# Kernel optimization log

Measured on AMD Instinct MI355X. Metric: run time of the kernel, lower is better.

## Reference

```python
import jax, jax.numpy as jnp
import numpy as np

B, C, H, W = 4, 128, 128, 128
HEADS, DHEAD = 8, C // 8
N = H * W
NEG_SLOPE = 0.2
LN_EPS = 1e-5


def _build_grid_edges(h, w):
    # 3x3 neighborhood including self (matches the torch double loop),
    # then append N extra self loops (add_self_loops in the module).
    rows, cols = [], []
    for r in range(h):
        for c in range(w):
            idx = r * w + c
            for dr in (-1, 0, 1):
                for dc in (-1, 0, 1):
                    nr, nc = r + dr, c + dc
                    if 0 <= nr < h and 0 <= nc < w:
                        rows.append(idx)
                        cols.append(nr * w + nc)
    rows += list(range(h * w))
    cols += list(range(h * w))
    return np.asarray(rows, np.int32), np.asarray(cols, np.int32)

_SRC_NP, _DST_NP = _build_grid_edges(H, W)  # PyG: messages flow src -> dst
SRC = jnp.asarray(_SRC_NP)
DST = jnp.asarray(_DST_NP)


def setup_inputs() -> dict:
    key = jax.random.key(0)
    ks = jax.random.split(key, 7)
    s_lin = 1.0 / np.sqrt(C)
    return {
        "x": jax.random.normal(ks[0], (B, C, H, W), jnp.float32),
        "W_lin": jax.random.normal(ks[1], (C, HEADS * DHEAD), jnp.float32) * s_lin,
        "att_src": jax.random.normal(ks[2], (HEADS, DHEAD), jnp.float32) * s_lin,
        "att_dst": jax.random.normal(ks[3], (HEADS, DHEAD), jnp.float32) * s_lin,
        "bias": jnp.zeros((C,), jnp.float32),
        "gamma": jnp.ones((C,), jnp.float32),
        "beta": jnp.zeros((C,), jnp.float32),
    }


def _gat_forward(x, W_lin, att_src, att_dst, bias, gamma, beta):
    b = x.shape[0]
    x_nodes = x.reshape(b, C, N).transpose(0, 2, 1)            # [B,N,C]
    xp = (x_nodes @ W_lin).reshape(b, N, HEADS, DHEAD)          # [B,N,H,D]
    a_src = jnp.einsum('bnhd,hd->bnh', xp, att_src)             # [B,N,H]
    a_dst = jnp.einsum('bnhd,hd->bnh', xp, att_dst)
    score = jax.nn.leaky_relu(a_src[:, SRC] + a_dst[:, DST], NEG_SLOPE)  # [B,E,H]

    def seg_softmax(s):  # [E,H] softmax over edges grouped by DST
        m = jax.ops.segment_max(s, DST, num_segments=N)
        e = jnp.exp(s - m[DST])
        den = jax.ops.segment_sum(e, DST, num_segments=N)
        return e / den[DST]

    alpha = jax.vmap(seg_softmax)(score)                        # [B,E,H]
    msg = xp[:, SRC] * alpha[..., None]                         # [B,E,H,D]
    agg = jax.vmap(lambda m: jax.ops.segment_sum(m, DST, num_segments=N))(msg)
    out = agg.reshape(b, N, C) + bias                           # GATConv bias
    out = jax.nn.elu(out)
    # LayerNorm over channel dim
    mu = out.mean(-1, keepdims=True)
    var = out.var(-1, keepdims=True)
    out = (out - mu) * jax.lax.rsqrt(var + LN_EPS) * gamma + beta
    return out.transpose(0, 2, 1).reshape(b, C, H, W)


def reference(x, W_lin, att_src, att_dst, bias, gamma, beta):
    return _gat_forward(x, W_lin, att_src, att_dst, bias, gamma, beta)
```

## Files before the change

kernel.cpp:

```cpp
#include <hip/hip_runtime.h>
#include <stdint.h>

#define BATCH  4
#define CCH    128
#define GRID_H 128
#define GRID_W 128
#define NNODE  (GRID_H*GRID_W)
#define NHEAD  8
#define DH     16
#define WPAD   68
#define WROWS  144

typedef __attribute__((ext_vector_type(8))) short short8;
typedef __attribute__((ext_vector_type(4))) float f32x4;
typedef __attribute__((ext_vector_type(4))) unsigned u32x4;

__device__ inline unsigned short f2bf(float f){
    unsigned u = __float_as_uint(f);
    return (unsigned short)((u + 0x7FFFu + ((u >> 16) & 1u)) >> 16);
}
__device__ inline unsigned packbf(float a, float b){
    return (unsigned)f2bf(a) | ((unsigned)f2bf(b) << 16);
}
__device__ inline float bflo(unsigned u){ return __uint_as_float(u << 16); }
__device__ inline float bfhi(unsigned u){ return __uint_as_float(u & 0xFFFF0000u); }

__global__ void kW(const float* __restrict__ Wl, const float* __restrict__ attS,
                   const float* __restrict__ attD, unsigned* __restrict__ Wb)
{
    __shared__ float Wa[8][16];
    const int t = threadIdx.x;
    const int cbase = blockIdx.x * 8;
    if (t < 128){
        int cl = t >> 4, j = t & 15;
        const float* av = (j < 8 ? attS + j*DH : attD + (j-8)*DH);
        const float* wr = Wl + (size_t)(cbase + cl)*CCH + (j & 7)*DH;
        float s = 0.f;
        #pragma unroll
        for (int d = 0; d < DH; ++d) s += wr[d]*av[d];
        Wa[cl][j] = s;
    }
    __syncthreads();
    for (int it = 0; it < 3; ++it){
        int flat = it*256 + t;
        if (flat < 576){
            int k2l = flat / 144, co = flat % 144;
            int k2 = blockIdx.x*4 + k2l;
            float w0, w1;
            if (co < CCH){
                w0 = Wl[(size_t)(2*k2)*CCH + co];
                w1 = Wl[(size_t)(2*k2+1)*CCH + co];
            } else {
                w0 = Wa[2*k2l][co-CCH];
                w1 = Wa[2*k2l+1][co-CCH];
            }
            Wb[co*WPAD + k2] = packbf(w0, w1);
        }
    }
}

__global__ __launch_bounds__(256, 3) void kA(
    const float* __restrict__ x, const unsigned* __restrict__ Wbg,
    unsigned short* __restrict__ xpb, float* __restrict__ scb)
{
    __shared__ __align__(16) unsigned WbL[WROWS*WPAD];

    const int t  = threadIdx.x;
    const int b  = blockIdx.y;
    const int n0 = blockIdx.x * 128;

    #pragma unroll
    for (int it = 0; it < 10; ++it){
        int f4 = it*256 + t;
        if (f4 < (WROWS*WPAD)/4)
            *(u32x4*)(&WbL[f4*4]) = *(const u32x4*)(Wbg + (size_t)f4*4);
    }
    __syncthreads();

    const int w = t >> 6, lane = t & 63;
    const int col = lane & 15, q = lane >> 4;
    const float* xb = x + (size_t)b*CCH*NNODE;
    const int nA = n0 + (2*w+0)*16 + col;
    const int nB = n0 + (2*w+1)*16 + col;

    f32x4 acc[2][9];
    #pragma unroll
    for (int mi = 0; mi < 2; ++mi)
        #pragma unroll
        for (int ct = 0; ct < 9; ++ct) acc[mi][ct] = (f32x4)(0.f);

    float xrA[8], xrB[8], x2A[8], x2B[8];
    #pragma unroll
    for (int j = 0; j < 8; ++j){
        const size_t co = (size_t)(q*8 + j)*NNODE;
        xrA[j] = xb[co + nA];
        xrB[j] = xb[co + nB];
    }

    union U { u32x4 u; short8 s; };
    #pragma unroll
    for (int kc = 0; kc < 4; ++kc){
        if (kc < 3){
            #pragma unroll
            for (int j = 0; j < 8; ++j){
                const size_t co = (size_t)((kc+1)*32 + q*8 + j)*NNODE;
                x2A[j] = xb[co + nA];
                x2B[j] = xb[co + nB];
            }
        }
        U fa0, fa1;
        #pragma unroll
        for (int i = 0; i < 4; ++i){
            fa0.u[i] = packbf(xrA[2*i], xrA[2*i+1]);
            fa1.u[i] = packbf(xrB[2*i], xrB[2*i+1]);
        }
        const int kof = kc*16 + q*4;
        #pragma unroll
        for (int ct = 0; ct < 9; ++ct){
            U fb; fb.u = *(const u32x4*)(&WbL[(ct*16+col)*WPAD + kof]);
            acc[0][ct] = __builtin_amdgcn_mfma_f32_16x16x32_bf16(fa0.s, fb.s, acc[0][ct], 0, 0, 0);
            acc[1][ct] = __builtin_amdgcn_mfma_f32_16x16x32_bf16(fa1.s, fb.s, acc[1][ct], 0, 0, 0);
        }
        #pragma unroll
        for (int j = 0; j < 8; ++j){ xrA[j] = x2A[j]; xrB[j] = x2B[j]; }
    }

    unsigned short* xr = xpb + (size_t)b*NNODE*CCH;
    float*          sr = scb + (size_t)b*NNODE*16;
    const int sidx = (col < 8) ? 2*col : 2*(col-8)+1;
    #pragma unroll
    for (int mi = 0; mi < 2; ++mi){
        #pragma unroll
        for (int r = 0; r < 4; ++r){
            const int n = n0 + (2*w+mi)*16 + q*4 + r;
            #pragma unroll
            for (int ct = 0; ct < 8; ++ct)
                xr[(size_t)n*CCH + ct*16 + col] = f2bf(acc[mi][ct][r]);
            sr[(size_t)n*16 + sidx] = acc[mi][8][r];
        }
    }
}

__device__ inline void kb_issue(int n, const float2* __restrict__ scB,
                                const uint2* __restrict__ xvb, int h, int l2,
                                int* vm, float2 sc[9], uint2 xv[9])
{
    const int rr = n >> 7, cc = n & 127;
    const bool vU = rr > 0, vD = rr < GRID_H-1, vL = cc > 0, vR = cc < GRID_W-1;
    int m = 0;
    #pragma unroll
    for (int e = 0; e < 9; ++e){
        const int dr = e/3 - 1, dc = e%3 - 1;
        const bool vr_ = (dr < 0) ? vU : (dr > 0 ? vD : true);
        const bool vc_ = (dc < 0) ? vL : (dc > 0 ? vR : true);
        const bool v = vr_ && vc_;
        const int src = v ? (n + dr*GRID_W + dc) : n;
        m |= ((int)v) << e;
        sc[e] = scB[src*8 + h];
        xv[e] = xvb[(size_t)src*32 + l2];
    }
    *vm = m;
}

__global__ __launch_bounds__(256, 3) void kB(
    const unsigned short* __restrict__ xpb, const float* __restrict__ scb,
    const float* __restrict__ bias, const float* __restrict__ gamma,
    const float* __restrict__ beta, float* __restrict__ out)
{
    __shared__ float outT[CCH][65];
    const int t = threadIdx.x, w = t >> 6, lane = t & 63;
    const int h2 = lane >> 5, l2 = lane & 31;
    const int b  = blockIdx.y;
    const int n0 = blockIdx.x * 64;
    const uint2*  xvb = (const uint2*)(xpb + (size_t)b*NNODE*CCH);
    const float2* scB = (const float2*)(scb + (size_t)b*NNODE*16);
    const int h = l2 >> 2;
    const f32x4 bi = *(const f32x4*)(bias  + 4*l2);
    const f32x4 ga = *(const f32x4*)(gamma + 4*l2);
    const f32x4 be = *(const f32x4*)(beta  + 4*l2);

    float2 scP[2][9]; uint2 xvP[2][9]; int vmP[2];

    #define NODE(i) (n0 + w*16 + 2*(i) + h2)
    kb_issue(NODE(0), scB, xvb, h, l2, &vmP[0], scP[0], xvP[0]);

    #pragma unroll
    for (int ii = 0; ii < 4; ++ii){
        #pragma unroll
        for (int ph = 0; ph < 2; ++ph){
            const int i = 2*ii + ph;
            const int cur = i & 1;
            if (i + 1 < 8)
                kb_issue(NODE(i+1), scB, xvb, h, l2, &vmP[cur^1], scP[cur^1], xvP[cur^1]);

            const int vm = vmP[cur];
            const float2* sc = scP[cur];
            const uint2*  xv = xvP[cur];
            const int nl = w*16 + 2*i + h2;

            const float ad = sc[4].y;
            float s[9], mx = -1e30f;
            #pragma unroll
            for (int e = 0; e < 9; ++e){
                float sv = sc[e].x + ad;
                sv = fmaxf(sv, 0.2f*sv);
                s[e] = ((vm >> e) & 1) ? sv : -1e30f;
                mx = fmaxf(mx, s[e]);
            }
            float wt[9], den = 0.f;
            #pragma unroll
            for (int e = 0; e < 9; ++e){
                float ex = __expf(s[e] - mx);
                ex = ((vm >> e) & 1) ? ex : 0.f;
                wt[e] = ex; den += ex;
            }
            den += wt[4];
            const float inv = __builtin_amdgcn_rcpf(den);

            float a0 = 0.f, a1 = 0.f, a2 = 0.f, a3 = 0.f;
            #pragma unroll
            for (int e = 0; e < 9; ++e){
                float f = wt[e] * inv;
                if (e == 4) f += f;
                a0 += f * bflo(xv[e].x);
                a1 += f * bfhi(xv[e].x);
                a2 += f * bflo(xv[e].y);
                a3 += f * bfhi(xv[e].y);
            }

            float o0 = a0 + bi[0], o1 = a1 + bi[1], o2 = a2 + bi[2], o3 = a3 + bi[3];
            o0 = o0 > 0.f ? o0 : __expf(o0) - 1.f;
            o1 = o1 > 0.f ? o1 : __expf(o1) - 1.f;
            o2 = o2 > 0.f ? o2 : __expf(o2) - 1.f;
            o3 = o3 > 0.f ? o3 : __expf(o3) - 1.f;

            float sm = (o0 + o1) + (o2 + o3);
            float sq = o0*o0 + o1*o1 + o2*o2 + o3*o3;
            #pragma unroll
            for (int off = 1; off <= 16; off <<= 1){
                sm += __shfl_xor(sm, off, 64);
                sq += __shfl_xor(sq, off, 64);
            }
            const float mu  = sm * (1.f/128.f);
            float var = sq * (1.f/128.f) - mu*mu;
            var = var < 0.f ? 0.f : var;
            const float rstd = __builtin_amdgcn_rsqf(var + 1e-5f);
            outT[4*l2+0][nl] = (o0 - mu)*rstd*ga[0] + be[0];
            outT[4*l2+1][nl] = (o1 - mu)*rstd*ga[1] + be[1];
            outT[4*l2+2][nl] = (o2 - mu)*rstd*ga[2] + be[2];
            outT[4*l2+3][nl] = (o3 - mu)*rstd*ga[3] + be[3];
        }
    }
    #undef NODE
    __syncthreads();

    float* ob = out + (size_t)b*CCH*NNODE + n0;
    #pragma unroll
    for (int it = 0; it < 32; ++it){
        int c = it*4 + w;
        ob[(size_t)c*NNODE + lane] = outT[c][lane];
    }
}

extern "C" void kernel_launch(void* const* d_in, const int* in_sizes, int n_in,
                              void* d_out, int out_size, void* d_ws, size_t ws_size,
                              hipStream_t stream)
{
    const float* x    = (const float*)d_in[0];
    const float* Wl   = (const float*)d_in[1];
    const float* attS = (const float*)d_in[2];
    const float* attD = (const float*)d_in[3];
    const float* bias = (const float*)d_in[4];
    const float* gamma= (const float*)d_in[5];
    const float* beta = (const float*)d_in[6];
    float* out = (float*)d_out;

    unsigned short* xpb = (unsigned short*)d_ws;
    float*          scb = (float*)(xpb + (size_t)BATCH*NNODE*CCH);
    unsigned*       Wb  = (unsigned*)(scb + (size_t)BATCH*NNODE*16);

    kW<<<dim3(16), 256, 0, stream>>>(Wl, attS, attD, Wb);
    kA<<<dim3(NNODE/128, BATCH), 256, 0, stream>>>(x, Wb, xpb, scb);
    kB<<<dim3(NNODE/64, BATCH), 256, 0, stream>>>(xpb, scb, bias, gamma, beta, out);
}
```

Baseline: 117.6 us.

## Fold weight prep into projection kernel, switch to fp16 with packed FMA, remap blocks

Removes the separate weight-preparation kernel. Each projection block now computes the attention-folded weights and packs them to bf16 in shared memory with a hardware packed-convert instruction. The intermediate projection is stored as fp16 and aggregated with packed half2 FMAs, and source and destination scores go into separate arrays. Blocks are remapped so row groups interleave across XCDs, aiming for better L2 locality of neighbouring rows. This saves one launch and some ALU work, but every block redoes the weight preparation, and accumulating in fp16 reduces precision.

New measurement: 119.7 us. No clear change (+1.8%).

```diff
diff --git a/kernel.cpp b/kernel.cpp
--- a/kernel.cpp
+++ b/kernel.cpp
@@ -1,4 +1,5 @@
 #include <hip/hip_runtime.h>
+#include <hip/hip_fp16.h>
 #include <stdint.h>
 
 #define BATCH  4
@@ -15,65 +16,72 @@
 typedef __attribute__((ext_vector_type(4))) float f32x4;
 typedef __attribute__((ext_vector_type(4))) unsigned u32x4;
 
-__device__ inline unsigned short f2bf(float f){
-    unsigned u = __float_as_uint(f);
-    return (unsigned short)((u + 0x7FFFu + ((u >> 16) & 1u)) >> 16);
-}
 __device__ inline unsigned packbf(float a, float b){
-    return (unsigned)f2bf(a) | ((unsigned)f2bf(b) << 16);
-}
-__device__ inline float bflo(unsigned u){ return __uint_as_float(u << 16); }
-__device__ inline float bfhi(unsigned u){ return __uint_as_float(u & 0xFFFF0000u); }
-
-__global__ void kW(const float* __restrict__ Wl, const float* __restrict__ attS,
-                   const float* __restrict__ attD, unsigned* __restrict__ Wb)
-{
-    __shared__ float Wa[8][16];
-    const int t = threadIdx.x;
-    const int cbase = blockIdx.x * 8;
-    if (t < 128){
-        int cl = t >> 4, j = t & 15;
-        const float* av = (j < 8 ? attS + j*DH : attD + (j-8)*DH);
-        const float* wr = Wl + (size_t)(cbase + cl)*CCH + (j & 7)*DH;
-        float s = 0.f;
-        #pragma unroll
-        for (int d = 0; d < DH; ++d) s += wr[d]*av[d];
-        Wa[cl][j] = s;
-    }
-    __syncthreads();
-    for (int it = 0; it < 3; ++it){
-        int flat = it*256 + t;
-        if (flat < 576){
-            int k2l = flat / 144, co = flat % 144;
-            int k2 = blockIdx.x*4 + k2l;
-            float w0, w1;
-            if (co < CCH){
-                w0 = Wl[(size_t)(2*k2)*CCH + co];
-                w1 = Wl[(size_t)(2*k2+1)*CCH + co];
-            } else {
-                w0 = Wa[2*k2l][co-CCH];
-                w1 = Wa[2*k2l+1][co-CCH];
-            }
-            Wb[co*WPAD + k2] = packbf(w0, w1);
-        }
-    }
+    unsigned r;
+    asm("v_cvt_pk_bf16_f32 %0, %1, %2" : "=v"(r) : "v"(a), "v"(b));
+    return r;
+}
+__device__ inline unsigned packhf(float a, float b){
+    unsigned r;
+    asm("v_cvt_pkrtz_f16_f32 %0, %1, %2" : "=v"(r) : "v"(a), "v"(b));
+    return r;
 }
 
 __global__ __launch_bounds__(256, 3) void kA(
-    const float* __restrict__ x, const unsigned* __restrict__ Wbg,
-    unsigned short* __restrict__ xpb, float* __restrict__ scb)
+    const float* __restrict__ x,   const float* __restrict__ Wl,
+    const float* __restrict__ attS, const float* __restrict__ attD,
+    __half* __restrict__ xpb, float* __restrict__ scS, float* __restrict__ scD)
 {
     __shared__ __align__(16) unsigned WbL[WROWS*WPAD];
+    __shared__ __align__(16) float att2[2*CCH];
+    __shared__ float Wa[CCH][17];
 
     const int t  = threadIdx.x;
     const int b  = blockIdx.y;
-    const int n0 = blockIdx.x * 128;
-
-    #pragma unroll
-    for (int it = 0; it < 10; ++it){
-        int f4 = it*256 + t;
-        if (f4 < (WROWS*WPAD)/4)
-            *(u32x4*)(&WbL[f4*4]) = *(const u32x4*)(Wbg + (size_t)f4*4);
+    const int bx = blockIdx.x;
+    const int row = (bx & 7)*16 + (bx >> 3);
+    const int n0  = row * GRID_W;
+
+    att2[t] = (t < CCH) ? attS[t] : attD[t - CCH];
+    __syncthreads();
+
+    {
+        const int j = t & 15;
+        f32x4 av[4];
+        #pragma unroll
+        for (int d4 = 0; d4 < 4; ++d4) av[d4] = *(const f32x4*)&att2[j*16 + d4*4];
+        #pragma unroll
+        for (int it = 0; it < 8; ++it){
+            const int k = it*16 + (t >> 4);
+            const float* wr = Wl + (size_t)k*CCH + (j & 7)*16;
+            float s = 0.f;
+            #pragma unroll
+            for (int d4 = 0; d4 < 4; ++d4){
+                f32x4 wv = *(const f32x4*)(wr + d4*4);
+                s += wv[0]*av[d4][0] + wv[1]*av[d4][1] + wv[2]*av[d4][2] + wv[3]*av[d4][3];
+            }
+            Wa[k][j] = s;
+        }
+    }
+    __syncthreads();
+
+    {
+        const int k2 = t >> 2, cb = t & 3;
+        const float* r0 = Wl + (size_t)(2*k2)*CCH + cb*32;
+        const float* r1 = r0 + CCH;
+        #pragma unroll
+        for (int i4 = 0; i4 < 8; ++i4){
+            f32x4 a = *(const f32x4*)(r0 + i4*4);
+            f32x4 c = *(const f32x4*)(r1 + i4*4);
+            #pragma unroll
+            for (int u = 0; u < 4; ++u)
+                WbL[(cb*32 + i4*4 + u)*WPAD + k2] = packbf(a[u], c[u]);
+        }
+        #pragma unroll
+        for (int jj = 0; jj < 4; ++jj){
+            const int j = cb*4 + jj;
+            WbL[(CCH + j)*WPAD + k2] = packbf(Wa[2*k2][j], Wa[2*k2+1][j]);
+        }
     }
     __syncthreads();
 
@@ -125,9 +133,9 @@
         for (int j = 0; j < 8; ++j){ xrA[j] = x2A[j]; xrB[j] = x2B[j]; }
     }
 
-    unsigned short* xr = xpb + (size_t)b*NNODE*CCH;
-    float*          sr = scb + (size_t)b*NNODE*16;
-    const int sidx = (col < 8) ? 2*col : 2*(col-8)+1;
+    __half* xr = xpb + (size_t)b*NNODE*CCH;
+    float*  sS = scS + (size_t)b*NNODE*NHEAD;
+    float*  sD = scD + (size_t)b*NNODE*NHEAD;
     #pragma unroll
     for (int mi = 0; mi < 2; ++mi){
         #pragma unroll
@@ -135,15 +143,18 @@
             const int n = n0 + (2*w+mi)*16 + q*4 + r;
             #pragma unroll
             for (int ct = 0; ct < 8; ++ct)
-                xr[(size_t)n*CCH + ct*16 + col] = f2bf(acc[mi][ct][r]);
-            sr[(size_t)n*16 + sidx] = acc[mi][8][r];
-        }
-    }
-}
-
-__device__ inline void kb_issue(int n, const float2* __restrict__ scB,
+                xr[(size_t)n*CCH + ct*16 + col] = __float2half(acc[mi][ct][r]);
+            const float v = acc[mi][8][r];
+            if (col < 8) sS[(size_t)n*NHEAD + col]     = v;
+            else         sD[(size_t)n*NHEAD + col - 8] = v;
+        }
+    }
+}
+
+__device__ inline void kb_issue(int n, const float* __restrict__ scSb,
+                                const float* __restrict__ scDb,
                                 const uint2* __restrict__ xvb, int h, int l2,
-                                int* vm, float2 sc[9], uint2 xv[9])
+                                int* vm, float aS[9], float* aD, uint2 xv[9])
 {
     const int rr = n >> 7, cc = n & 127;
     const bool vU = rr > 0, vD = rr < GRID_H-1, vL = cc > 0, vR = cc < GRID_W-1;
@@ -156,14 +167,16 @@
         const bool v = vr_ && vc_;
         const int src = v ? (n + dr*GRID_W + dc) : n;
         m |= ((int)v) << e;
-        sc[e] = scB[src*8 + h];
+        aS[e] = scSb[src*NHEAD + h];
         xv[e] = xvb[(size_t)src*32 + l2];
     }
+    *aD = scDb[n*NHEAD + h];
     *vm = m;
 }
 
 __global__ __launch_bounds__(256, 3) void kB(
-    const unsigned short* __restrict__ xpb, const float* __restrict__ scb,
+    const __half* __restrict__ xpb, const float* __restrict__ scS,
+    const float* __restrict__ scD,
     const float* __restrict__ bias, const float* __restrict__ gamma,
     const float* __restrict__ beta, float* __restrict__ out)
 {
@@ -171,18 +184,23 @@
     const int t = threadIdx.x, w = t >> 6, lane = t & 63;
     const int h2 = lane >> 5, l2 = lane & 31;
     const int b  = blockIdx.y;
-    const int n0 = blockIdx.x * 64;
-    const uint2*  xvb = (const uint2*)(xpb + (size_t)b*NNODE*CCH);
-    const float2* scB = (const float2*)(scb + (size_t)b*NNODE*16);
+    const int bx = blockIdx.x;
+    const int xcd = bx & 7, rest = bx >> 3;
+    const int hlf = rest & 1, rowin = rest >> 1;
+    const int n0  = (xcd*16 + rowin)*GRID_W + hlf*64;
+
+    const uint2* xvb  = (const uint2*)(xpb + (size_t)b*NNODE*CCH);
+    const float* scSb = scS + (size_t)b*NNODE*NHEAD;
+    const float* scDb = scD + (size_t)b*NNODE*NHEAD;
     const int h = l2 >> 2;
     const f32x4 bi = *(const f32x4*)(bias  + 4*l2);
     const f32x4 ga = *(const f32x4*)(gamma + 4*l2);
     const f32x4 be = *(const f32x4*)(beta  + 4*l2);
 
-    float2 scP[2][9]; uint2 xvP[2][9]; int vmP[2];
+    float aSP[2][9]; uint2 xvP[2][9]; float aDP[2]; int vmP[2];
 
     #define NODE(i) (n0 + w*16 + 2*(i) + h2)
-    kb_issue(NODE(0), scB, xvb, h, l2, &vmP[0], scP[0], xvP[0]);
+    kb_issue(NODE(0), scSb, scDb, xvb, h, l2, &vmP[0], aSP[0], &aDP[0], xvP[0]);
 
     #pragma unroll
     for (int ii = 0; ii < 4; ++ii){
@@ -191,18 +209,19 @@
             const int i = 2*ii + ph;
             const int cur = i & 1;
             if (i + 1 < 8)
-                kb_issue(NODE(i+1), scB, xvb, h, l2, &vmP[cur^1], scP[cur^1], xvP[cur^1]);
+                kb_issue(NODE(i+1), scSb, scDb, xvb, h, l2,
+                         &vmP[cur^1], aSP[cur^1], &aDP[cur^1], xvP[cur^1]);
 
             const int vm = vmP[cur];
-            const float2* sc = scP[cur];
+            const float* aS = aSP[cur];
             const uint2*  xv = xvP[cur];
+            const float ad = aDP[cur];
             const int nl = w*16 + 2*i + h2;
 
-            const float ad = sc[4].y;
             float s[9], mx = -1e30f;
             #pragma unroll
             for (int e = 0; e < 9; ++e){
-                float sv = sc[e].x + ad;
+                float sv = aS[e] + ad;
                 sv = fmaxf(sv, 0.2f*sv);
                 s[e] = ((vm >> e) & 1) ? sv : -1e30f;
                 mx = fmaxf(mx, s[e]);
@@ -217,16 +236,20 @@
             den += wt[4];
             const float inv = __builtin_amdgcn_rcpf(den);
 
-            float a0 = 0.f, a1 = 0.f, a2 = 0.f, a3 = 0.f;
+            union HU { unsigned u; __half2 h; };
+            HU a01, a23; a01.u = 0u; a23.u = 0u;
             #pragma unroll
             for (int e = 0; e < 9; ++e){
                 float f = wt[e] * inv;
                 if (e == 4) f += f;
-                a0 += f * bflo(xv[e].x);
-                a1 += f * bfhi(xv[e].x);
-                a2 += f * bflo(xv[e].y);
-                a3 += f * bfhi(xv[e].y);
-            }
+                HU hf; hf.u = packhf(f, f);
+                HU lo; lo.u = xv[e].x;
+                HU hi; hi.u = xv[e].y;
+                a01.h = __hfma2(hf.h, lo.h, a01.h);
+                a23.h = __hfma2(hf.h, hi.h, a23.h);
+            }
+            const float a0 = __low2float(a01.h), a1 = __high2float(a01.h);
+            const float a2 = __low2float(a23.h), a3 = __high2float(a23.h);
 
             float o0 = a0 + bi[0], o1 = a1 + bi[1], o2 = a2 + bi[2], o3 = a3 + bi[3];
             o0 = o0 > 0.f ? o0 : __expf(o0) - 1.f;
@@ -275,11 +298,10 @@
     const float* beta = (const float*)d_in[6];
     float* out = (float*)d_out;
 
-    unsigned short* xpb = (unsigned short*)d_ws;
-    float*          scb = (float*)(xpb + (size_t)BATCH*NNODE*CCH);
-    unsigned*       Wb  = (unsigned*)(scb + (size_t)BATCH*NNODE*16);
-
-    kW<<<dim3(16), 256, 0, stream>>>(Wl, attS, attD, Wb);
-    kA<<<dim3(NNODE/128, BATCH), 256, 0, stream>>>(x, Wb, xpb, scb);
-    kB<<<dim3(NNODE/64, BATCH), 256, 0, stream>>>(xpb, scb, bias, gamma, beta, out);
-}
+    __half* xpb = (__half*)d_ws;
+    float*  scS = (float*)((char*)d_ws + (size_t)BATCH*NNODE*CCH*2);
+    float*  scD = scS + (size_t)BATCH*NNODE*NHEAD;
+
+    kA<<<dim3(NNODE/128, BATCH), 256, 0, stream>>>(x, Wl, attS, attD, xpb, scS, scD);
+    kB<<<dim3(NNODE/64,  BATCH), 256, 0, stream>>>(xpb, scS, scD, bias, gamma, beta, out);
+}
```
